# Kernel tuning notes

Measured on AMD Instinct MI355X. Metric: run time of the kernel, lower is better.

The kernel has to match this reference:

```python
import jax, jax.numpy as jnp
import numpy as np

NUM_HEADS = 32
MICRO_BATCHES = 2
TOP_K = 2
LN_EPS = 1e-5


def _mha(x, scale, bias, wq, wk, wv, wo):
    # Pre-LN multi-head self-attention with residual (RealSelfAttention).
    B, S, D = x.shape
    H = NUM_HEADS
    hd = D // H
    res = x
    mu = jnp.mean(x, axis=-1, keepdims=True)
    xc = x - mu
    var = jnp.mean(xc * xc, axis=-1, keepdims=True)
    xn = xc / jnp.sqrt(var + LN_EPS) * scale + bias
    q = (xn @ wq.T).reshape(B, S, H, hd).transpose(0, 2, 1, 3)
    k = (xn @ wk.T).reshape(B, S, H, hd).transpose(0, 2, 1, 3)
    v = (xn @ wv.T).reshape(B, S, H, hd).transpose(0, 2, 1, 3)
    scores = jnp.einsum('bhqd,bhkd->bhqk', q, k) * (1.0 / np.sqrt(hd).astype(np.float32))
    attn = jax.nn.softmax(scores, axis=-1)
    o = jnp.einsum('bhqk,bhkd->bhqd', attn, v).transpose(0, 2, 1, 3).reshape(B, S, D)
    return o @ wo.T + res


def setup_inputs() -> dict:
    key = jax.random.key(0)
    D, E, F = 1024, 8, 4096
    B, S = 4, 1024
    ks = jax.random.split(key, 16)
    w = lambda k, shape: (jax.random.normal(k, shape, dtype=jnp.float32) * 0.02)
    return {
        'x': jax.random.normal(ks[0], (B, S, D), dtype=jnp.float32),
        'ln1_scale': jnp.ones((D,), jnp.float32),
        'ln1_bias': jnp.zeros((D,), jnp.float32),
        'wq1': w(ks[1], (D, D)), 'wk1': w(ks[2], (D, D)),
        'wv1': w(ks[3], (D, D)), 'wo1': w(ks[4], (D, D)),
        'gate_w': w(ks[5], (E, D)),
        'exp_w1': w(ks[6], (E, F, D)), 'exp_b1': jnp.zeros((E, F), jnp.float32),
        'exp_w2': w(ks[7], (E, D, F)), 'exp_b2': jnp.zeros((E, D), jnp.float32),
        'ln2_scale': jnp.ones((D,), jnp.float32),
        'ln2_bias': jnp.zeros((D,), jnp.float32),
        'wq2': w(ks[8], (D, D)), 'wk2': w(ks[9], (D, D)),
        'wv2': w(ks[10], (D, D)), 'wo2': w(ks[11], (D, D)),
    }


def reference(x, ln1_scale, ln1_bias, wq1, wk1, wv1, wo1, gate_w,
              exp_w1, exp_b1, exp_w2, exp_b2,
              ln2_scale, ln2_bias, wq2, wk2, wv2, wo2):
    B, S, D = x.shape
    E = exp_w1.shape[0]
    # PreOps: attention layer L (per-sample, so full-batch apply == per-microbatch apply)
    y = _mha(x, ln1_scale, ln1_bias, wq1, wk1, wv1, wo1)
    # Gate: logits + top-k indices computed in source but never applied to tokens.
    flat = y.reshape(B * S, D)
    logits = flat @ gate_w.T
    _ = jax.lax.top_k(logits, TOP_K)  # indices unused downstream (faithful to source)
    # Dispatch (all_to_all on 1 device == identity): per-microbatch flat tokens are
    # chunked equally across local experts.
    T = (B // MICRO_BATCHES) * S            # tokens per microbatch
    toks = y.reshape(MICRO_BATCHES, E, T // E, D)
    h = jax.nn.gelu(jnp.einsum('metd,efd->metf', toks, exp_w1) + exp_b1[None, :, None, :],
                    approximate=False)
    eo = jnp.einsum('metf,edf->metd', h, exp_w2) + exp_b2[None, :, None, :]
    # Combine (identity) + PostOps: attention layer L+1
    z = eo.reshape(B, S, D)
    out = _mha(z, ln2_scale, ln2_bias, wq2, wk2, wv2, wo2)
    return out
```

## Files before the change

kernel.cpp:

```cpp
#include <hip/hip_runtime.h>

typedef __attribute__((ext_vector_type(8))) short bf16x8;
typedef __attribute__((ext_vector_type(4))) float f32x4;
typedef __attribute__((ext_vector_type(4))) short short4v;

#define DEV __device__ __forceinline__

DEV short f2bf(float f) {
  union { float f; unsigned u; } x; x.f = f;
  unsigned r = x.u + 0x7fffu + ((x.u >> 16) & 1u);
  return (short)(r >> 16);
}

#define GL2LDS16(g, l) __builtin_amdgcn_global_load_lds(                      \
    (const __attribute__((address_space(1))) void*)(g),                       \
    (__attribute__((address_space(3))) void*)(l), 16, 0, 0)

__global__ __launch_bounds__(256) void k_cast_bf16(const float* __restrict__ s,
                                                   short* __restrict__ d, int n4) {
  int i = blockIdx.x * 256 + threadIdx.x;
  if (i >= n4) return;
  float4 v = ((const float4*)s)[i];
  short4v o;
  o[0] = f2bf(v.x); o[1] = f2bf(v.y); o[2] = f2bf(v.z); o[3] = f2bf(v.w);
  ((short4v*)d)[i] = o;
}

__global__ __launch_bounds__(256)
void k_ln(const float* __restrict__ X, const float* __restrict__ G,
          const float* __restrict__ Bi, short* __restrict__ Y) {
  const int row = blockIdx.x, t = threadIdx.x;
  const float4 v = ((const float4*)(X + (size_t)row * 1024))[t];
  float s = v.x + v.y + v.z + v.w;
  float s2 = v.x * v.x + v.y * v.y + v.z * v.z + v.w * v.w;
#pragma unroll
  for (int m = 1; m < 64; m <<= 1) { s += __shfl_xor(s, m); s2 += __shfl_xor(s2, m); }
  __shared__ float rs[4], rq[4];
  const int w = t >> 6, lane = t & 63;
  if (lane == 0) { rs[w] = s; rq[w] = s2; }
  __syncthreads();
  s = rs[0] + rs[1] + rs[2] + rs[3];
  s2 = rq[0] + rq[1] + rq[2] + rq[3];
  const float mu = s * (1.f / 1024.f);
  const float var = s2 * (1.f / 1024.f) - mu * mu;
  const float rstd = rsqrtf(var + 1e-5f);
  const float4 g = ((const float4*)G)[t];
  const float4 bi = ((const float4*)Bi)[t];
  short4v o;
  o[0] = f2bf((v.x - mu) * rstd * g.x + bi.x);
  o[1] = f2bf((v.y - mu) * rstd * g.y + bi.y);
  o[2] = f2bf((v.z - mu) * rstd * g.z + bi.z);
  o[3] = f2bf((v.w - mu) * rstd * g.w + bi.w);
  ((short4v*)(Y + (size_t)row * 1024))[t] = o;
}

template <int EPI, int EXPERT, int BN, int BF32>
__global__ __launch_bounds__(256)
void k_gemm_bt(const short* __restrict__ A, const void* __restrict__ Btv,
               void* __restrict__ Cv, const float* __restrict__ Res,
               const float* __restrict__ Bias, int M, int N, int K, int xt) {
  constexpr int NF = BN / 32;
  constexpr int BR = BN / 64;
  __shared__ __attribute__((aligned(16))) short As[2][128 * 32];
  __shared__ __attribute__((aligned(16))) short Bs[2][BN * 32];
  const int tid = threadIdx.x;
  const int w = tid >> 6, lane = tid & 63;
  const int r16 = lane & 15, kg = lane >> 4;
  const int wr = w >> 1, wc = w & 1;

  const int bid = blockIdx.x;
  int bx;
  size_t rowBase, bOff = 0, biasOff = 0;
  if constexpr (EXPERT) {
    int e = bid & 7, mb = (bid >> 3) & 1, by = (bid >> 4) & 1;
    bx = bid >> 5;
    rowBase = (size_t)by * 128 + (size_t)(mb * 8 + e) * 256;
    bOff = (size_t)e * N * K;
    biasOff = (size_t)e * N;
  } else {
    int y7 = bid & 7, r = bid >> 3;
    bx = r % xt;
    rowBase = (size_t)(y7 + 8 * (r / xt)) * 128;
  }
  const size_t col0 = (size_t)bx * BN;
  const short* Ab = A + rowBase * K;
  const short* Bb16 = (const short*)Btv + bOff + col0 * K;
  const float* Bb32 = (const float*)Btv + bOff + col0 * K;

  f32x4 acc[4][NF] = {};
  float4 nb[BR][2];

  auto stageA = [&](int buf, int k0) {
#pragma unroll
    for (int i = 0; i < 2; ++i) {
      int c = (i * 4 + w) * 64 + lane;
      int row = c >> 2;
      int sl = (c & 3) ^ (row & 3);
      GL2LDS16(Ab + (size_t)row * K + k0 + sl * 8, (char*)As[buf] + (size_t)(i * 4 + w) * 1024);
    }
  };
  auto stageB16 = [&](int buf, int k0) {
#pragma unroll
    for (int i = 0; i < BR; ++i) {
      int c = (i * 4 + w) * 64 + lane;
      int row = c >> 2;
      int sl = (c & 3) ^ (row & 3);
      GL2LDS16(Bb16 + (size_t)row * K + k0 + sl * 8, (char*)Bs[buf] + (size_t)(i * 4 + w) * 1024);
    }
  };
  auto loadB32 = [&](int k0) {
#pragma unroll
    for (int i = 0; i < BR; ++i) {
      int c = (i * 4 + w) * 64 + lane;
      int row = c >> 2;
      int sl = (c & 3) ^ (row & 3);
      const float* src = Bb32 + (size_t)row * K + k0 + sl * 8;
      nb[i][0] = *(const float4*)src;
      nb[i][1] = *(const float4*)(src + 4);
    }
  };
  auto writeB32 = [&](int buf) {
#pragma unroll
    for (int i = 0; i < BR; ++i) {
      union { short s[8]; bf16x8 v; } o;
      o.s[0] = f2bf(nb[i][0].x); o.s[1] = f2bf(nb[i][0].y);
      o.s[2] = f2bf(nb[i][0].z); o.s[3] = f2bf(nb[i][0].w);
      o.s[4] = f2bf(nb[i][1].x); o.s[5] = f2bf(nb[i][1].y);
      o.s[6] = f2bf(nb[i][1].z); o.s[7] = f2bf(nb[i][1].w);
      *(bf16x8*)((char*)Bs[buf] + (size_t)(i * 4 + w) * 1024 + (size_t)lane * 16) = o.v;
    }
  };

  stageA(0, 0);
  if constexpr (BF32) { loadB32(0); writeB32(0); } else { stageB16(0, 0); }
  __syncthreads();
  int cur = 0;
  for (int k0 = 0; k0 < K; k0 += 32) {
    const bool nxt = (k0 + 32 < K);
    if (nxt) {
      stageA(cur ^ 1, k0 + 32);
      if constexpr (BF32) loadB32(k0 + 32); else stageB16(cur ^ 1, k0 + 32);
    }
    bf16x8 af[4], bg[NF];
#pragma unroll
    for (int m = 0; m < 4; ++m) {
      int row = wr * 64 + m * 16 + r16;
      af[m] = *(const bf16x8*)(As[cur] + row * 32 + (kg ^ (row & 3)) * 8);
    }
#pragma unroll
    for (int n = 0; n < NF; ++n) {
      int row = wc * (BN / 2) + n * 16 + r16;
      bg[n] = *(const bf16x8*)(Bs[cur] + row * 32 + (kg ^ (row & 3)) * 8);
    }
#pragma unroll
    for (int m = 0; m < 4; ++m)
#pragma unroll
      for (int n = 0; n < NF; ++n)
        acc[m][n] = __builtin_amdgcn_mfma_f32_16x16x32_bf16(af[m], bg[n], acc[m][n], 0, 0, 0);
    if (nxt) { if constexpr (BF32) writeB32(cur ^ 1); }
    __syncthreads();
    cur ^= 1;
  }

#pragma unroll
  for (int m = 0; m < 4; ++m) {
    size_t grow0 = rowBase + wr * 64 + m * 16 + kg * 4;
#pragma unroll
    for (int n = 0; n < NF; ++n) {
      size_t gcol = col0 + wc * (BN / 2) + n * 16 + r16;
#pragma unroll
      for (int r = 0; r < 4; ++r) {
        size_t idx = (grow0 + r) * (size_t)N + gcol;
        float v = acc[m][n][r];
        if constexpr (EPI == 1 || EPI == 4) v += Res[idx];
        if constexpr (EPI == 2 || EPI == 3) v += Bias[biasOff + gcol];
        if constexpr (EPI == 2) v = 0.5f * v * (1.f + erff(v * 0.70710678118654752f));
        if constexpr (EPI <= 2) ((short*)Cv)[idx] = f2bf(v);
        else                    ((float*)Cv)[idx] = v;
      }
    }
  }
  (void)M;
}

__global__ __launch_bounds__(256, 3)
void k_attn(const short* __restrict__ QKV, short* __restrict__ O) {
  const int bid = blockIdx.x;
  const int qt = bid >> 7, h = bid & 31, b = (bid >> 5) & 3;
  const int tid = threadIdx.x, w = tid >> 6, lane = tid & 63;
  const int r16 = lane & 15, kg = lane >> 4;

  __shared__ __attribute__((aligned(16))) short Kl[2][128 * 32];
  __shared__ __attribute__((aligned(16))) short Vt[2][32 * 128];
  __shared__ __attribute__((aligned(16))) short Pl[4][16 * 128];

  const size_t tb = (size_t)b * 1024;
  const int qbase = qt * 128 + w * 32;

  bf16x8 aq[2];
#pragma unroll
  for (int f = 0; f < 2; ++f)
    aq[f] = *(const bf16x8*)(QKV + (tb + qbase + f * 16 + r16) * 3072 + h * 32 + kg * 8);

  f32x4 acc[2][2] = {};
  float lreg[2][4] = {};
  const float scale = 0.17677669529663687f;

  auto stageK = [&](int bid2, int kc) {
#pragma unroll
    for (int i = 0; i < 2; ++i) {
      int c = (i * 4 + w) * 64 + lane;
      int row = c >> 2;
      int sl = (c & 3) ^ (row & 3);
      GL2LDS16(QKV + (tb + kc * 128 + row) * 3072 + 1024 + h * 32 + sl * 8,
               (char*)Kl[bid2] + (size_t)(i * 4 + w) * 1024);
    }
  };

  stageK(0, 0);
  {
    int c0 = tid,        vr0 = c0 >> 2, d00 = (c0 & 3) * 8;
    int c1 = 256 + tid,  vr1 = c1 >> 2, d01 = (c1 & 3) * 8;
    bf16x8 v0 = *(const bf16x8*)(QKV + (tb + vr0) * 3072 + 2048 + h * 32 + d00);
    bf16x8 v1 = *(const bf16x8*)(QKV + (tb + vr1) * 3072 + 2048 + h * 32 + d01);
#pragma unroll
    for (int j = 0; j < 8; ++j) {
      int da = d00 + j, db = d01 + j;
      Vt[0][((da * 128 + vr0) ^ ((da & 7) << 3))] = v0[j];
      Vt[0][((db * 128 + vr1) ^ ((db & 7) << 3))] = v1[j];
    }
  }
  __syncthreads();

  int bi = 0;
  for (int kc = 0; kc < 8; ++kc) {
    bf16x8 nv0, nv1;
    int nvr0 = 0, nd0 = 0, nvr1 = 0, nd1 = 0;
    if (kc < 7) {
      stageK(bi ^ 1, kc + 1);
      const short* Vg = QKV + (tb + (size_t)(kc + 1) * 128) * 3072 + 2048 + h * 32;
      int c0 = tid;       nvr0 = c0 >> 2; nd0 = (c0 & 3) * 8;
      int c1 = 256 + tid; nvr1 = c1 >> 2; nd1 = (c1 & 3) * 8;
      nv0 = *(const bf16x8*)(Vg + (size_t)nvr0 * 3072 + nd0);
      nv1 = *(const bf16x8*)(Vg + (size_t)nvr1 * 3072 + nd1);
    }

    f32x4 s[2][8];
#pragma unroll
    for (int kt = 0; kt < 8; ++kt) {
      int row = kt * 16 + r16;
      bf16x8 bk = *(const bf16x8*)(Kl[bi] + row * 32 + (kg ^ (row & 3)) * 8);
      f32x4 zz = {0.f, 0.f, 0.f, 0.f};
      s[0][kt] = __builtin_amdgcn_mfma_f32_16x16x32_bf16(aq[0], bk, zz, 0, 0, 0);
      s[1][kt] = __builtin_amdgcn_mfma_f32_16x16x32_bf16(aq[1], bk, zz, 0, 0, 0);
    }

#pragma unroll
    for (int f = 0; f < 2; ++f)
#pragma unroll
      for (int r = 0; r < 4; ++r) {
        float sum = 0.f;
#pragma unroll
        for (int kt = 0; kt < 8; ++kt) {
          float p = __expf(s[f][kt][r] * scale);
          s[f][kt][r] = p;
          sum += p;
        }
#pragma unroll
        for (int m = 1; m < 16; m <<= 1) sum += __shfl_xor(sum, m);
        lreg[f][r] += sum;
      }

    short* P = Pl[w];
#pragma unroll
    for (int f = 0; f < 2; ++f) {
#pragma unroll
      for (int kt = 0; kt < 8; ++kt)
#pragma unroll
        for (int r = 0; r < 4; ++r) {
          int row = kg * 4 + r;
          P[((row * 128 + kt * 16 + r16) ^ ((row & 7) << 3))] = f2bf(s[f][kt][r]);
        }
#pragma unroll
      for (int ks = 0; ks < 4; ++ks) {
        bf16x8 pa = *(const bf16x8*)(P + ((r16 * 128 + ks * 32 + kg * 8) ^ ((r16 & 7) << 3)));
#pragma unroll
        for (int dt = 0; dt < 2; ++dt) {
          int vrow = dt * 16 + r16;
          bf16x8 bv = *(const bf16x8*)(Vt[bi] + ((vrow * 128 + ks * 32 + kg * 8) ^ ((vrow & 7) << 3)));
          acc[f][dt] = __builtin_amdgcn_mfma_f32_16x16x32_bf16(pa, bv, acc[f][dt], 0, 0, 0);
        }
      }
    }

    if (kc < 7) {
#pragma unroll
      for (int j = 0; j < 8; ++j) {
        int da = nd0 + j, db = nd1 + j;
        Vt[bi ^ 1][((da * 128 + nvr0) ^ ((da & 7) << 3))] = nv0[j];
        Vt[bi ^ 1][((db * 128 + nvr1) ^ ((db & 7) << 3))] = nv1[j];
      }
    }

    __syncthreads();
    bi ^= 1;
  }

#pragma unroll
  for (int f = 0; f < 2; ++f)
#pragma unroll
    for (int r = 0; r < 4; ++r) {
      float inv = 1.f / lreg[f][r];
      size_t qrow = tb + qbase + f * 16 + kg * 4 + r;
#pragma unroll
      for (int dt = 0; dt < 2; ++dt)
        O[qrow * 1024 + h * 32 + dt * 16 + r16] = f2bf(acc[f][dt][r] * inv);
    }
}

extern "C" void kernel_launch(void* const* d_in, const int* in_sizes, int n_in,
                              void* d_out, int out_size, void* d_ws, size_t ws_size,
                              hipStream_t stream) {
  const float* x    = (const float*)d_in[0];
  const float* ln1s = (const float*)d_in[1];
  const float* ln1b = (const float*)d_in[2];
  const float* wq1  = (const float*)d_in[3];
  const float* wk1  = (const float*)d_in[4];
  const float* wv1  = (const float*)d_in[5];
  const float* wo1  = (const float*)d_in[6];
  const float* ew1  = (const float*)d_in[8];
  const float* eb1  = (const float*)d_in[9];
  const float* ew2  = (const float*)d_in[10];
  const float* eb2  = (const float*)d_in[11];
  const float* ln2s = (const float*)d_in[12];
  const float* ln2b = (const float*)d_in[13];
  const float* wq2  = (const float*)d_in[14];
  const float* wk2  = (const float*)d_in[15];
  const float* wv2  = (const float*)d_in[16];
  const float* wo2  = (const float*)d_in[17];

  char* ws = (char*)d_ws;
  size_t off = 0;
  auto alloc = [&](size_t bytes) {
    char* p = ws + off;
    off += (bytes + 255) & ~(size_t)255;
    return p;
  };
  short* wqkv1b = (short*)alloc(3072ull * 1024 * 2);
  short* wo1b   = (short*)alloc(1024ull * 1024 * 2);
  short* wqkv2b = (short*)alloc(3072ull * 1024 * 2);
  short* wo2b   = (short*)alloc(1024ull * 1024 * 2);
  short* xnb    = (short*)alloc(4096ull * 1024 * 2);
  short* qkvo   = (short*)alloc(4096ull * 4096 * 2);
  short* ybf    = (short*)alloc(4096ull * 1024 * 2);
  float* zf     = (float*)alloc(4096ull * 1024 * 4);
  (void)ws_size; (void)in_sizes; (void)n_in; (void)out_size;

  short* QKV = qkvo;
  short* Ob  = qkvo + 4096ull * 3072;
  short* hb  = qkvo;

  auto cast = [&](const float* s, short* d, size_t n) {
    int n4 = (int)(n / 4);
    k_cast_bf16<<<(n4 + 255) / 256, 256, 0, stream>>>(s, d, n4);
  };
  cast(wq1, wqkv1b,           1048576);
  cast(wk1, wqkv1b + 1048576, 1048576);
  cast(wv1, wqkv1b + 2097152, 1048576);
  cast(wo1, wo1b,             1048576);
  cast(wq2, wqkv2b,           1048576);
  cast(wk2, wqkv2b + 1048576, 1048576);
  cast(wv2, wqkv2b + 2097152, 1048576);
  cast(wo2, wo2b,             1048576);

  k_ln<<<4096, 256, 0, stream>>>(x, ln1s, ln1b, xnb);
  k_gemm_bt<0, 0, 128, 0><<<768, 256, 0, stream>>>(xnb, wqkv1b, QKV, nullptr, nullptr, 4096, 3072, 1024, 24);
  k_attn<<<1024, 256, 0, stream>>>(QKV, Ob);
  k_gemm_bt<1, 0, 64, 0><<<512, 256, 0, stream>>>(Ob, wo1b, ybf, x, nullptr, 4096, 1024, 1024, 16);
  k_gemm_bt<2, 1, 128, 1><<<1024, 256, 0, stream>>>(ybf, ew1, hb, nullptr, eb1, 256, 4096, 1024, 0);
  k_gemm_bt<3, 1, 64, 1><<<512, 256, 0, stream>>>(hb, ew2, zf, nullptr, eb2, 256, 1024, 4096, 0);
  k_ln<<<4096, 256, 0, stream>>>(zf, ln2s, ln2b, xnb);
  k_gemm_bt<0, 0, 128, 0><<<768, 256, 0, stream>>>(xnb, wqkv2b, QKV, nullptr, nullptr, 4096, 3072, 1024, 24);
  k_attn<<<1024, 256, 0, stream>>>(QKV, Ob);
  k_gemm_bt<4, 0, 64, 0><<<512, 256, 0, stream>>>(Ob, wo2b, (float*)d_out, zf, nullptr, 4096, 1024, 1024, 16);
}
```

Before: 543.1 us.

## Stage fp32 weights directly to LDS and convert to bf16 at fragment load

For GEMMs whose B operand is fp32, the register round-trip (global load to registers, software bf16 rounding, LDS store) is replaced by asynchronous global-to-LDS copies of the raw fp32 tile. The conversion to bf16 now happens after each LDS fragment read, using the HIP bf16 intrinsic. This removes register pressure and the explicit LDS write from the main loop so B loads overlap with MFMA like the A loads do. The cost is twice the LDS footprint and read bandwidth for B, plus conversion work repeated by every wave that reads the same fragment.

```diff
diff --git a/kernel.cpp b/kernel.cpp
--- a/kernel.cpp
+++ b/kernel.cpp
@@ -1,4 +1,5 @@
 #include <hip/hip_runtime.h>
+#include <hip/hip_bf16.h>
 
 typedef __attribute__((ext_vector_type(8))) short bf16x8;
 typedef __attribute__((ext_vector_type(4))) float f32x4;
@@ -10,6 +11,21 @@
   union { float f; unsigned u; } x; x.f = f;
   unsigned r = x.u + 0x7fffu + ((x.u >> 16) & 1u);
   return (short)(r >> 16);
+}
+
+DEV short f2bf_hw(float f) {
+  union { __hip_bfloat16 h; short s; } c;
+  c.h = __float2bfloat16(f);
+  return c.s;
+}
+
+DEV bf16x8 cvt8(f32x4 a, f32x4 b) {
+  union { short s[8]; bf16x8 v; } o;
+  o.s[0] = f2bf_hw(a[0]); o.s[1] = f2bf_hw(a[1]);
+  o.s[2] = f2bf_hw(a[2]); o.s[3] = f2bf_hw(a[3]);
+  o.s[4] = f2bf_hw(b[0]); o.s[5] = f2bf_hw(b[1]);
+  o.s[6] = f2bf_hw(b[2]); o.s[7] = f2bf_hw(b[3]);
+  return o.v;
 }
 
 #define GL2LDS16(g, l) __builtin_amdgcn_global_load_lds(                      \
@@ -62,7 +78,7 @@
   constexpr int NF = BN / 32;
   constexpr int BR = BN / 64;
   __shared__ __attribute__((aligned(16))) short As[2][128 * 32];
-  __shared__ __attribute__((aligned(16))) short Bs[2][BN * 32];
+  __shared__ __attribute__((aligned(16))) char Braw[2][BN * 32 * (BF32 ? 4 : 2)];
   const int tid = threadIdx.x;
   const int w = tid >> 6, lane = tid & 63;
   const int r16 = lane & 15, kg = lane >> 4;
@@ -88,9 +104,8 @@
   const float* Bb32 = (const float*)Btv + bOff + col0 * K;
 
   f32x4 acc[4][NF] = {};
-  float4 nb[BR][2];
-
-  auto stageA = [&](int buf, int k0) {
+
+  auto stage = [&](int buf, int k0) {
 #pragma unroll
     for (int i = 0; i < 2; ++i) {
       int c = (i * 4 + w) * 64 + lane;
@@ -98,66 +113,59 @@
       int sl = (c & 3) ^ (row & 3);
       GL2LDS16(Ab + (size_t)row * K + k0 + sl * 8, (char*)As[buf] + (size_t)(i * 4 + w) * 1024);
     }
+    if constexpr (BF32) {
+#pragma unroll
+      for (int i = 0; i < NF; ++i) {
+        int c = i * 256 + tid;
+        int row = c >> 3;
+        int sl = (c & 7) ^ (row & 7);
+        GL2LDS16(Bb32 + (size_t)row * K + k0 + sl * 4, (char*)Braw[buf] + (size_t)(i * 4 + w) * 1024);
+      }
+    } else {
+#pragma unroll
+      for (int i = 0; i < BR; ++i) {
+        int c = i * 256 + tid;
+        int row = c >> 2;
+        int sl = (c & 3) ^ (row & 3);
+        GL2LDS16(Bb16 + (size_t)row * K + k0 + sl * 8, (char*)Braw[buf] + (size_t)(i * 4 + w) * 1024);
+      }
+    }
   };
-  auto stageB16 = [&](int buf, int k0) {
-#pragma unroll
-    for (int i = 0; i < BR; ++i) {
-      int c = (i * 4 + w) * 64 + lane;
-      int row = c >> 2;
-      int sl = (c & 3) ^ (row & 3);
-      GL2LDS16(Bb16 + (size_t)row * K + k0 + sl * 8, (char*)Bs[buf] + (size_t)(i * 4 + w) * 1024);
-    }
-  };
-  auto loadB32 = [&](int k0) {
-#pragma unroll
-    for (int i = 0; i < BR; ++i) {
-      int c = (i * 4 + w) * 64 + lane;
-      int row = c >> 2;
-      int sl = (c & 3) ^ (row & 3);
-      const float* src = Bb32 + (size_t)row * K + k0 + sl * 8;
-      nb[i][0] = *(const float4*)src;
-      nb[i][1] = *(const float4*)(src + 4);
-    }
-  };
-  auto writeB32 = [&](int buf) {
-#pragma unroll
-    for (int i = 0; i < BR; ++i) {
-      union { short s[8]; bf16x8 v; } o;
-      o.s[0] = f2bf(nb[i][0].x); o.s[1] = f2bf(nb[i][0].y);
-      o.s[2] = f2bf(nb[i][0].z); o.s[3] = f2bf(nb[i][0].w);
-      o.s[4] = f2bf(nb[i][1].x); o.s[5] = f2bf(nb[i][1].y);
-      o.s[6] = f2bf(nb[i][1].z); o.s[7] = f2bf(nb[i][1].w);
-      *(bf16x8*)((char*)Bs[buf] + (size_t)(i * 4 + w) * 1024 + (size_t)lane * 16) = o.v;
-    }
-  };
-
-  stageA(0, 0);
-  if constexpr (BF32) { loadB32(0); writeB32(0); } else { stageB16(0, 0); }
+
+  stage(0, 0);
   __syncthreads();
   int cur = 0;
   for (int k0 = 0; k0 < K; k0 += 32) {
-    const bool nxt = (k0 + 32 < K);
-    if (nxt) {
-      stageA(cur ^ 1, k0 + 32);
-      if constexpr (BF32) loadB32(k0 + 32); else stageB16(cur ^ 1, k0 + 32);
-    }
+    if (k0 + 32 < K) stage(cur ^ 1, k0 + 32);
     bf16x8 af[4], bg[NF];
 #pragma unroll
     for (int m = 0; m < 4; ++m) {
       int row = wr * 64 + m * 16 + r16;
       af[m] = *(const bf16x8*)(As[cur] + row * 32 + (kg ^ (row & 3)) * 8);
     }
-#pragma unroll
-    for (int n = 0; n < NF; ++n) {
-      int row = wc * (BN / 2) + n * 16 + r16;
-      bg[n] = *(const bf16x8*)(Bs[cur] + row * 32 + (kg ^ (row & 3)) * 8);
+    if constexpr (BF32) {
+      const float* Bf = (const float*)Braw[cur];
+#pragma unroll
+      for (int n = 0; n < NF; ++n) {
+        int row = wc * (BN / 2) + n * 16 + r16;
+        int s0 = (2 * kg) ^ (row & 7), s1 = (2 * kg + 1) ^ (row & 7);
+        f32x4 fa = *(const f32x4*)(Bf + row * 32 + s0 * 4);
+        f32x4 fb = *(const f32x4*)(Bf + row * 32 + s1 * 4);
+        bg[n] = cvt8(fa, fb);
+      }
+    } else {
+      const short* Bh = (const short*)Braw[cur];
+#pragma unroll
+      for (int n = 0; n < NF; ++n) {
+        int row = wc * (BN / 2) + n * 16 + r16;
+        bg[n] = *(const bf16x8*)(Bh + row * 32 + (kg ^ (row & 3)) * 8);
+      }
     }
 #pragma unroll
     for (int m = 0; m < 4; ++m)
 #pragma unroll
       for (int n = 0; n < NF; ++n)
         acc[m][n] = __builtin_amdgcn_mfma_f32_16x16x32_bf16(af[m], bg[n], acc[m][n], 0, 0, 0);
-    if (nxt) { if constexpr (BF32) writeB32(cur ^ 1); }
     __syncthreads();
     cur ^= 1;
   }
```

Result: no change. 539.0 us (-0.8%).
